# Kernel tuning notes

Hardware: AMD Instinct MI355X
Metric: run time of the kernel (lower is better)

The kernel has to match this reference:

```python
import jax, jax.numpy as jnp
import numpy as np

IN_FF = 7  # joints
MASK = np.ones(9, dtype=np.float32)  # [P(3), RPY sin/cos (6)]


def _mlp(x, params):
    # params: list of (W, b); sigmoid after every layer except the last (predict)
    h = x
    for W, b in params[:-1]:
        h = jax.nn.sigmoid(h @ W + b)
    W, b = params[-1]
    return h @ W + b


def _rpy_head(x, params):
    # FeedForwardNet_RPY forward: y -> [sin(y0), cos(y1)], angle = atan2(sin, cos)
    y = _mlp(x, params)
    s = jnp.sin(y[..., 0])
    c = jnp.cos(y[..., 1])
    ang = jnp.arctan2(s, c)
    return jnp.stack([s, c, ang], axis=-1)  # (..., 3)


def setup_inputs():
    key = jax.random.key(0)
    ks = jax.random.split(key, 26)
    m = 16384
    d = {"x": jax.random.normal(ks[0], (m, 2 * IN_FF), jnp.float32)}

    def lin(k, fi, fo, name, i):
        k1, k2 = jax.random.split(k)
        lim = 1.0 / np.sqrt(fi)  # torch Linear default init
        d[name + "_W" + str(i)] = jax.random.uniform(k1, (fi, fo), jnp.float32, -lim, lim)
        d[name + "_b" + str(i)] = jax.random.uniform(k2, (fo,), jnp.float32, -lim, lim)

    idx = 1
    for name, dims in [("pos", [7, 512, 512, 3]), ("roll", [7, 256, 256, 2]),
                       ("pitch", [7, 256, 256, 2]), ("yaw", [7, 256, 256, 2])]:
        for i in range(3):
            lin(ks[idx], dims[i], dims[i + 1], name, i)
            idx += 1
    return d


def _forward(x, pos_p, roll_p, pitch_p, yaw_p):
    mask = jnp.asarray(MASK)
    M_P, M_RPY = mask[:3], mask[3:]
    q, qdot = x[:, :IN_FF], x[:, IN_FF:]

    # position net: forward + per-sample Jacobian (exact, replaces the autograd loop)
    P = _mlp(q, pos_p)                                          # (m, 3)
    J_P = jax.vmap(jax.jacfwd(lambda z: _mlp(z, pos_p)))(q)     # (m, 3, 7)
    vel = jnp.einsum("moi,mi->mo", J_P, qdot)                   # bmm(J_P, jointVels)
    P = P * M_P
    vel = vel * M_P

    heads = []
    for p in (roll_p, pitch_p, yaw_p):
        f = lambda z, p=p: _rpy_head(z, p)
        y = f(q)                                # (m, 3): [sin, cos, angle]
        J = jax.vmap(jax.jacfwd(f))(q)          # (m, 3, 7)
        v = jnp.einsum("moi,mi->mo", J[:, :2, :], qdot)  # (m, 2)
        heads.append((y, J, v))
    (yR, JR, vR), (yPi, JPi, vPi), (yY, JY, vY) = heads

    # order: [roll_sin, pitch_sin, yaw_sin, roll_cos, pitch_cos, yaw_cos]
    RPY = jnp.stack([yR[:, 0], yPi[:, 0], yY[:, 0], yR[:, 1], yPi[:, 1], yY[:, 1]], axis=1) * M_RPY
    vel_RPY = jnp.stack([vR[:, 0], vPi[:, 0], vY[:, 0], vR[:, 1], vPi[:, 1], vY[:, 1]], axis=1) * M_RPY
    J_RPY = jnp.stack([JR[:, 0], JPi[:, 0], JY[:, 0], JR[:, 1], JPi[:, 1], JY[:, 1]], axis=1)  # (m,6,7)

    out = jnp.concatenate([P, RPY, vel, vel_RPY], axis=1)            # (m, 18)
    J_tot = jnp.concatenate([J_P, J_RPY], axis=1)                    # (m, 9, 7)
    out_angles = jnp.concatenate([P, yR[:, 2:3], yPi[:, 2:3], yY[:, 2:3]], axis=1)       # (m, 6)
    J_tot_angles = jnp.concatenate([J_P, JR[:, 2:3], JPi[:, 2:3], JY[:, 2:3]], axis=1)   # (m, 6, 7)
    return out, J_tot, out_angles, J_tot_angles


def reference(x, pos_W0, pos_b0, pos_W1, pos_b1, pos_W2, pos_b2,
              roll_W0, roll_b0, roll_W1, roll_b1, roll_W2, roll_b2,
              pitch_W0, pitch_b0, pitch_W1, pitch_b1, pitch_W2, pitch_b2,
              yaw_W0, yaw_b0, yaw_W1, yaw_b1, yaw_W2, yaw_b2):
    pos_p = [(pos_W0, pos_b0), (pos_W1, pos_b1), (pos_W2, pos_b2)]
    roll_p = [(roll_W0, roll_b0), (roll_W1, roll_b1), (roll_W2, roll_b2)]
    pitch_p = [(pitch_W0, pitch_b0), (pitch_W1, pitch_b1), (pitch_W2, pitch_b2)]
    yaw_p = [(yaw_W0, yaw_b0), (yaw_W1, yaw_b1), (yaw_W2, yaw_b2)]
    return _forward(x, pos_p, roll_p, pitch_p, yaw_p)
```

## Files before the change

kernel.cpp:

```cpp
#include <hip/hip_runtime.h>
#include <math.h>

typedef __attribute__((ext_vector_type(8))) short short8;
typedef __attribute__((ext_vector_type(4))) float floatx4;

__device__ __forceinline__ float sig(float z) {
    return __builtin_amdgcn_rcpf(1.0f + __expf(-z));
}

__device__ __forceinline__ unsigned short f2bf(float f) {
    unsigned u = __float_as_uint(f);
    u = (u + 0x7FFFu + ((u >> 16) & 1u)) >> 16;
    return (unsigned short)u;
}

#if __has_builtin(__builtin_amdgcn_cvt_pk_bf16_f32)
typedef __attribute__((ext_vector_type(2))) short short2v;
__device__ __forceinline__ unsigned int pack2bf(float a, float b) {
    short2v r = __builtin_amdgcn_cvt_pk_bf16_f32(a, b);
    return *(unsigned int*)&r;
}
#else
__device__ __forceinline__ unsigned int pack2bf(float a, float b) {
    unsigned ua = __float_as_uint(a), ub = __float_as_uint(b);
    ua += 0x7FFFu + ((ua >> 16) & 1u);
    ub += 0x7FFFu + ((ub >> 16) & 1u);
    return __builtin_amdgcn_perm(ub, ua, 0x07060302);
}
#endif

__global__ void convert_all(const float* __restrict__ s0, const float* __restrict__ s1,
                            const float* __restrict__ s2, const float* __restrict__ s3,
                            unsigned short* __restrict__ ws) {
    int idx = blockIdx.x * 256 + threadIdx.x;
    const float* src; unsigned short* dst; int H, logH, local;
    if (idx < 262144) { src = s0; dst = ws; H = 512; logH = 9; local = idx; }
    else {
        int r = idx - 262144; int m = r >> 16; local = r & 65535;
        H = 256; logH = 8;
        src = (m == 0) ? s1 : (m == 1) ? s2 : s3;
        dst = ws + 262144 + m * 65536;
    }
    int n = local & (H - 1), k = local >> logH;
    int KT = H >> 5;
    int blk = (n >> 4) * KT + (k >> 5);
    int lane = ((k >> 3) & 3) * 16 + (n & 15);
    int j = k & 7;
    dst[(blk * 64 + lane) * 8 + j] = f2bf(src[local]);
}

struct PosS {
    float B0[512], B1[512], W2[1536];
    float Q[8][8], Qd[8][8];
    float Acc[4][64][3], Sum[64][3];
};
struct RpyS {
    float B0[256], B1[256], W2[512];
    float Q[16][8], Qd[16][8];
    float Acc[4][128][2], Sum[128][2];
};

__global__ __launch_bounds__(256, 2)
void fused_mfma(const float* __restrict__ x,
                const float* __restrict__ pW0, const float* __restrict__ pb0,
                const float* __restrict__ pb1,
                const float* __restrict__ pW2, const float* __restrict__ pb2,
                const float* __restrict__ rW0_, const float* __restrict__ rb0_,
                const float* __restrict__ rb1_,
                const float* __restrict__ rW2_, const float* __restrict__ rb2_,
                const float* __restrict__ piW0, const float* __restrict__ pib0,
                const float* __restrict__ pib1,
                const float* __restrict__ piW2, const float* __restrict__ pib2,
                const float* __restrict__ yW0, const float* __restrict__ yb0,
                const float* __restrict__ yb1,
                const float* __restrict__ yW2, const float* __restrict__ yb2,
                const unsigned short* __restrict__ wsBase,
                float* __restrict__ out, int ns)
{
    extern __shared__ unsigned short sA[];
    __shared__ union { PosS p; RpyS r; } sU;

    const int tid = threadIdx.x;
    const int f = blockIdx.x;
    const int g = f / 5, r5 = f % 5;
    const size_t JTOT = (size_t)ns * 18, OUTA = (size_t)ns * 81, JANG = (size_t)ns * 87;
    const floatx4 z4 = {0.f, 0.f, 0.f, 0.f};
    const int w = tid >> 6, lane = tid & 63;
    const int quad = lane >> 4, col = lane & 15;
    const int srcl = lane & 47;

    if (r5 < 2) {
        const int m0 = (g * 2 + r5) * 8;
        const unsigned short* wsW1 = wsBase;

        if (tid < 128) {
            ((float4*)sU.p.B0)[tid] = ((const float4*)pb0)[tid];
            ((float4*)sU.p.B1)[tid] = ((const float4*)pb1)[tid];
        }
        for (int i = tid; i < 384; i += 256) ((float4*)sU.p.W2)[i] = ((const float4*)pW2)[i];
        if (tid < 112) {
            int m = tid / 14, c = tid % 14;
            float v = x[(m0 + m) * 14 + c];
            if (c < 7) sU.p.Q[m][c] = v; else sU.p.Qd[m][c - 7] = v;
        }
        __syncthreads();

        const float4* W04 = (const float4*)pW0;
        #pragma unroll
        for (int t = 0; t < 2; ++t) {
            int item = tid + t * 256;
            int s = item >> 6, k8 = item & 63;
            float q[7], w0v[7][8];
            #pragma unroll
            for (int i = 0; i < 7; i++) {
                q[i] = sU.p.Q[s][i];
                float4 a = W04[i * 128 + k8 * 2], b4 = W04[i * 128 + k8 * 2 + 1];
                w0v[i][0]=a.x; w0v[i][1]=a.y; w0v[i][2]=a.z; w0v[i][3]=a.w;
                w0v[i][4]=b4.x; w0v[i][5]=b4.y; w0v[i][6]=b4.z; w0v[i][7]=b4.w;
            }
            float hv[8], dv[8];
            #pragma unroll
            for (int jj = 0; jj < 8; jj++) {
                float z = sU.p.B0[k8 * 8 + jj];
                #pragma unroll
                for (int i = 0; i < 7; i++) z = fmaf(q[i], w0v[i][jj], z);
                float h = sig(z);
                hv[jj] = h; dv[jj] = h - h * h;
            }
            int kt = k8 >> 2, kq = k8 & 3, sw = kt & 7;
            int rr0 = s * 8;
            {
                uint4 v;
                v.x = pack2bf(hv[0], hv[1]); v.y = pack2bf(hv[2], hv[3]);
                v.z = pack2bf(hv[4], hv[5]); v.w = pack2bf(hv[6], hv[7]);
                *(uint4*)&sA[((rr0 >> 4) * 16 + kt) * 512 + ((kq * 16 + (rr0 & 15)) ^ sw) * 8] = v;
            }
            #pragma unroll
            for (int i = 0; i < 7; i++) {
                int rr = rr0 + 1 + i;
                uint4 v;
                v.x = pack2bf(dv[0] * w0v[i][0], dv[1] * w0v[i][1]);
                v.y = pack2bf(dv[2] * w0v[i][2], dv[3] * w0v[i][3]);
                v.z = pack2bf(dv[4] * w0v[i][4], dv[5] * w0v[i][5]);
                v.w = pack2bf(dv[6] * w0v[i][6], dv[7] * w0v[i][7]);
                *(uint4*)&sA[((rr >> 4) * 16 + kt) * 512 + ((kq * 16 + (rr & 15)) ^ sw) * 8] = v;
            }
        }
        __syncthreads();

        floatx4 acc[4][8];
        #pragma unroll
        for (int rt = 0; rt < 4; rt++)
            #pragma unroll
            for (int ct = 0; ct < 8; ct++) acc[rt][ct] = z4;

        const short8* bbase = (const short8*)wsW1 + (size_t)(w * 8 * 16) * 64 + lane;
        short8 bufA[8], bufB[8];
        #pragma unroll
        for (int ct = 0; ct < 8; ++ct) bufA[ct] = bbase[(ct * 16) * 64];

        for (int kt2 = 0; kt2 < 16; kt2 += 2) {
            #pragma unroll
            for (int ct = 0; ct < 8; ++ct) bufB[ct] = bbase[(ct * 16 + kt2 + 1) * 64];
            {
                const int kt = kt2, sw = kt & 7;
                short8 afr[4];
                #pragma unroll
                for (int rt = 0; rt < 4; ++rt)
                    afr[rt] = *(const short8*)&sA[(rt * 16 + kt) * 512 + (lane ^ sw) * 8];
                #pragma unroll
                for (int ct = 0; ct < 8; ++ct)
                    #pragma unroll
                    for (int rt = 0; rt < 4; ++rt)
                        acc[rt][ct] = __builtin_amdgcn_mfma_f32_16x16x32_bf16(afr[rt], bufA[ct], acc[rt][ct], 0, 0, 0);
            }
            if (kt2 + 2 < 16) {
                #pragma unroll
                for (int ct = 0; ct < 8; ++ct) bufA[ct] = bbase[(ct * 16 + kt2 + 2) * 64];
            }
            {
                const int kt = kt2 + 1, sw = kt & 7;
                short8 afr[4];
                #pragma unroll
                for (int rt = 0; rt < 4; ++rt)
                    afr[rt] = *(const short8*)&sA[(rt * 16 + kt) * 512 + (lane ^ sw) * 8];
                #pragma unroll
                for (int ct = 0; ct < 8; ++ct)
                    #pragma unroll
                    for (int rt = 0; rt < 4; ++rt)
                        acc[rt][ct] = __builtin_amdgcn_mfma_f32_16x16x32_bf16(afr[rt], bufB[ct], acc[rt][ct], 0, 0, 0);
            }
        }

        float ep[4][4][3];
        #pragma unroll
        for (int a = 0; a < 4; a++) for (int b = 0; b < 4; b++) for (int c = 0; c < 3; c++) ep[a][b][c] = 0.f;

        #pragma unroll
        for (int ct = 0; ct < 8; ++ct) {
            const int n = w * 128 + ct * 16 + col;
            const float b1n = sU.p.B1[n];
            const float w20 = sU.p.W2[n * 3], w21 = sU.p.W2[n * 3 + 1], w22 = sU.p.W2[n * 3 + 2];
            #pragma unroll
            for (int rt = 0; rt < 4; ++rt) {
                float z2c = __shfl(acc[rt][ct][0], srcl);
                float h2 = sig(z2c + b1n);
                float d2 = h2 - h2 * h2;
                #pragma unroll
                for (int r = 0; r < 4; ++r) {
                    float gg = ((quad & 1) == 0 && r == 0) ? h2 : d2 * acc[rt][ct][r];
                    ep[rt][r][0] = fmaf(gg, w20, ep[rt][r][0]);
                    ep[rt][r][1] = fmaf(gg, w21, ep[rt][r][1]);
                    ep[rt][r][2] = fmaf(gg, w22, ep[rt][r][2]);
                }
            }
        }

        #pragma unroll
        for (int mask = 1; mask <= 8; mask <<= 1)
            #pragma unroll
            for (int a = 0; a < 4; a++)
                #pragma unroll
                for (int b = 0; b < 4; b++)
                    #pragma unroll
                    for (int c = 0; c < 3; c++)
                        ep[a][b][c] += __shfl_xor(ep[a][b][c], mask);
        if (col == 0) {
            #pragma unroll
            for (int rt = 0; rt < 4; ++rt)
                #pragma unroll
                for (int r = 0; r < 4; ++r) {
                    int row = rt * 16 + quad * 4 + r;
                    sU.p.Acc[w][row][0] = ep[rt][r][0];
                    sU.p.Acc[w][row][1] = ep[rt][r][1];
                    sU.p.Acc[w][row][2] = ep[rt][r][2];
                }
        }
        __syncthreads();

        if (tid < 192) {
            int row = tid / 3, j = tid % 3;
            float v = sU.p.Acc[0][row][j] + sU.p.Acc[1][row][j] + sU.p.Acc[2][row][j] + sU.p.Acc[3][row][j];
            int s = row >> 3, i = row & 7;
            size_t M = m0 + s;
            if (i == 0) { v += pb2[j]; out[M * 18 + j] = v; out[OUTA + M * 6 + j] = v; }
            else        { out[JTOT + M * 63 + j * 7 + (i - 1)] = v;
                          out[JANG + M * 42 + j * 7 + (i - 1)] = v; }
            sU.p.Sum[row][j] = v;
        }
        __syncthreads();
        if (tid < 24) {
            int s = tid / 3, j = tid % 3;
            float vel = 0.f;
            #pragma unroll
            for (int i = 0; i < 7; i++) vel = fmaf(sU.p.Sum[s * 8 + 1 + i][j], sU.p.Qd[s][i], vel);
            out[(size_t)(m0 + s) * 18 + 9 + j] = vel;
        }
    } else {
        const int h = r5 - 2;
        const int m0 = g * 16;
        const float* W0 = (h == 0) ? rW0_ : (h == 1) ? piW0 : yW0;
        const float* b0 = (h == 0) ? rb0_ : (h == 1) ? pib0 : yb0;
        const float* b1 = (h == 0) ? rb1_ : (h == 1) ? pib1 : yb1;
        const float* W2 = (h == 0) ? rW2_ : (h == 1) ? piW2 : yW2;
        const float* b2 = (h == 0) ? rb2_ : (h == 1) ? pib2 : yb2;
        const unsigned short* wsW1 = wsBase + 262144 + h * 65536;

        if (tid < 64) {
            ((float4*)sU.r.B0)[tid] = ((const float4*)b0)[tid];
            ((float4*)sU.r.B1)[tid] = ((const float4*)b1)[tid];
        } else if (tid < 192) {
            ((float4*)sU.r.W2)[tid - 64] = ((const float4*)W2)[tid - 64];
        }
        if (tid < 224) {
            int m = tid / 14, c = tid % 14;
            float v = x[(m0 + m) * 14 + c];
            if (c < 7) sU.r.Q[m][c] = v; else sU.r.Qd[m][c - 7] = v;
        }
        __syncthreads();

        const float4* W04 = (const float4*)W0;
        #pragma unroll
        for (int t = 0; t < 2; ++t) {
            int item = tid + t * 256;
            int s = item >> 5, k8 = item & 31;
            float q[7], w0v[7][8];
            #pragma unroll
            for (int i = 0; i < 7; i++) {
                q[i] = sU.r.Q[s][i];
                float4 a = W04[i * 64 + k8 * 2], b4 = W04[i * 64 + k8 * 2 + 1];
                w0v[i][0]=a.x; w0v[i][1]=a.y; w0v[i][2]=a.z; w0v[i][3]=a.w;
                w0v[i][4]=b4.x; w0v[i][5]=b4.y; w0v[i][6]=b4.z; w0v[i][7]=b4.w;
            }
            float hv[8], dv[8];
            #pragma unroll
            for (int jj = 0; jj < 8; jj++) {
                float z = sU.r.B0[k8 * 8 + jj];
                #pragma unroll
                for (int i = 0; i < 7; i++) z = fmaf(q[i], w0v[i][jj], z);
                float hh = sig(z);
                hv[jj] = hh; dv[jj] = hh - hh * hh;
            }
            int kt = k8 >> 2, kq = k8 & 3, sw = kt & 7;
            int rr0 = s * 8;
            {
                uint4 v;
                v.x = pack2bf(hv[0], hv[1]); v.y = pack2bf(hv[2], hv[3]);
                v.z = pack2bf(hv[4], hv[5]); v.w = pack2bf(hv[6], hv[7]);
                *(uint4*)&sA[((rr0 >> 4) * 8 + kt) * 512 + ((kq * 16 + (rr0 & 15)) ^ sw) * 8] = v;
            }
            #pragma unroll
            for (int i = 0; i < 7; i++) {
                int rr = rr0 + 1 + i;
                uint4 v;
                v.x = pack2bf(dv[0] * w0v[i][0], dv[1] * w0v[i][1]);
                v.y = pack2bf(dv[2] * w0v[i][2], dv[3] * w0v[i][3]);
                v.z = pack2bf(dv[4] * w0v[i][4], dv[5] * w0v[i][5]);
                v.w = pack2bf(dv[6] * w0v[i][6], dv[7] * w0v[i][7]);
                *(uint4*)&sA[((rr >> 4) * 8 + kt) * 512 + ((kq * 16 + (rr & 15)) ^ sw) * 8] = v;
            }
        }
        __syncthreads();

        floatx4 acc[8][4];
        #pragma unroll
        for (int rt = 0; rt < 8; rt++)
            #pragma unroll
            for (int ct = 0; ct < 4; ct++) acc[rt][ct] = z4;

        const short8* bbase = (const short8*)wsW1 + (size_t)(w * 4 * 8) * 64 + lane;
        short8 bufA[4], bufB[4];
        #pragma unroll
        for (int ct = 0; ct < 4; ++ct) bufA[ct] = bbase[(ct * 8) * 64];

        for (int kt2 = 0; kt2 < 8; kt2 += 2) {
            #pragma unroll
            for (int ct = 0; ct < 4; ++ct) bufB[ct] = bbase[(ct * 8 + kt2 + 1) * 64];
            {
                const int kt = kt2, sw = kt & 7;
                short8 afr[8];
                #pragma unroll
                for (int rt = 0; rt < 8; ++rt)
                    afr[rt] = *(const short8*)&sA[(rt * 8 + kt) * 512 + (lane ^ sw) * 8];
                #pragma unroll
                for (int ct = 0; ct < 4; ++ct)
                    #pragma unroll
                    for (int rt = 0; rt < 8; ++rt)
                        acc[rt][ct] = __builtin_amdgcn_mfma_f32_16x16x32_bf16(afr[rt], bufA[ct], acc[rt][ct], 0, 0, 0);
            }
            if (kt2 + 2 < 8) {
                #pragma unroll
                for (int ct = 0; ct < 4; ++ct) bufA[ct] = bbase[(ct * 8 + kt2 + 2) * 64];
            }
            {
                const int kt = kt2 + 1, sw = kt & 7;
                short8 afr[8];
                #pragma unroll
                for (int rt = 0; rt < 8; ++rt)
                    afr[rt] = *(const short8*)&sA[(rt * 8 + kt) * 512 + (lane ^ sw) * 8];
                #pragma unroll
                for (int ct = 0; ct < 4; ++ct)
                    #pragma unroll
                    for (int rt = 0; rt < 8; ++rt)
                        acc[rt][ct] = __builtin_amdgcn_mfma_f32_16x16x32_bf16(afr[rt], bufB[ct], acc[rt][ct], 0, 0, 0);
            }
        }

        float ep[8][4][2];
        #pragma unroll
        for (int a = 0; a < 8; a++) for (int b = 0; b < 4; b++) for (int c = 0; c < 2; c++) ep[a][b][c] = 0.f;

        #pragma unroll
        for (int ct = 0; ct < 4; ++ct) {
            const int n = w * 64 + ct * 16 + col;
            const float b1n = sU.r.B1[n];
            const float w20 = sU.r.W2[n * 2], w21 = sU.r.W2[n * 2 + 1];
            #pragma unroll
            for (int rt = 0; rt < 8; ++rt) {
                float z2c = __shfl(acc[rt][ct][0], srcl);
                float h2 = sig(z2c + b1n);
                float d2 = h2 - h2 * h2;
                #pragma unroll
                for (int r = 0; r < 4; ++r) {
                    float gg = ((quad & 1) == 0 && r == 0) ? h2 : d2 * acc[rt][ct][r];
                    ep[rt][r][0] = fmaf(gg, w20, ep[rt][r][0]);
                    ep[rt][r][1] = fmaf(gg, w21, ep[rt][r][1]);
                }
            }
        }

        #pragma unroll
        for (int mask = 1; mask <= 8; mask <<= 1)
            #pragma unroll
            for (int a = 0; a < 8; a++)
                #pragma unroll
                for (int b = 0; b < 4; b++)
                    #pragma unroll
                    for (int c = 0; c < 2; c++)
                        ep[a][b][c] += __shfl_xor(ep[a][b][c], mask);
        if (col == 0) {
            #pragma unroll
            for (int rt = 0; rt < 8; ++rt)
                #pragma unroll
                for (int r = 0; r < 4; ++r) {
                    int row = rt * 16 + quad * 4 + r;
                    sU.r.Acc[w][row][0] = ep[rt][r][0];
                    sU.r.Acc[w][row][1] = ep[rt][r][1];
                }
        }
        __syncthreads();

        if (tid < 256) {
            int row = tid >> 1, j = tid & 1;
            float v = sU.r.Acc[0][row][j] + sU.r.Acc[1][row][j] + sU.r.Acc[2][row][j] + sU.r.Acc[3][row][j];
            if ((row & 7) == 0) v += b2[j];
            sU.r.Sum[row][j] = v;
        }
        __syncthreads();

        if (tid < 16) {
            int s = tid;
            size_t M = m0 + s;
            float y0 = sU.r.Sum[s * 8][0], y1 = sU.r.Sum[s * 8][1];
            float sv = sinf(y0), cv = cosf(y1);
            out[M * 18 + 3 + h] = sv;
            out[M * 18 + 6 + h] = cv;
            out[OUTA + M * 6 + 3 + h] = atan2f(sv, cv);
            float f0 = cosf(y0), f1 = -sinf(y1);
            float inv = __builtin_amdgcn_rcpf(fmaf(sv, sv, cv * cv));
            float v0 = 0.f, v1 = 0.f;
            #pragma unroll
            for (int i = 0; i < 7; i++) {
                float r0 = f0 * sU.r.Sum[s * 8 + 1 + i][0];
                float r1 = f1 * sU.r.Sum[s * 8 + 1 + i][1];
                out[JTOT + M * 63 + (3 + h) * 7 + i] = r0;
                out[JTOT + M * 63 + (6 + h) * 7 + i] = r1;
                out[JANG + M * 42 + (3 + h) * 7 + i] = (cv * r0 - sv * r1) * inv;
                v0 = fmaf(r0, sU.r.Qd[s][i], v0);
                v1 = fmaf(r1, sU.r.Qd[s][i], v1);
            }
            out[M * 18 + 12 + h] = v0;
            out[M * 18 + 15 + h] = v1;
        }
    }
}

extern "C" void kernel_launch(void* const* d_in, const int* in_sizes, int n_in,
                              void* d_out, int out_size, void* d_ws, size_t ws_size,
                              hipStream_t stream) {
    (void)n_in; (void)out_size; (void)ws_size;
    const float* x = (const float*)d_in[0];
    float* out = (float*)d_out;
    unsigned short* ws = (unsigned short*)d_ws;
    const int ns = in_sizes[0] / 14;

    convert_all<<<dim3(1792), 256, 0, stream>>>(
        (const float*)d_in[3], (const float*)d_in[9],
        (const float*)d_in[15], (const float*)d_in[21], ws);

    fused_mfma<<<dim3((ns / 8 / 2) * 5), 256, 65536, stream>>>(
        x,
        (const float*)d_in[1],  (const float*)d_in[2],  (const float*)d_in[4],
        (const float*)d_in[5],  (const float*)d_in[6],
        (const float*)d_in[7],  (const float*)d_in[8],  (const float*)d_in[10],
        (const float*)d_in[11], (const float*)d_in[12],
        (const float*)d_in[13], (const float*)d_in[14], (const float*)d_in[16],
        (const float*)d_in[17], (const float*)d_in[18],
        (const float*)d_in[19], (const float*)d_in[20], (const float*)d_in[22],
        (const float*)d_in[23], (const float*)d_in[24],
        ws, out, ns);
}
```

Measured before the change: 341.7 us.

## Process two sample tiles per block with double-buffered inputs, read W2 from global

Each block now loops over two consecutive sample tiles instead of one, halving the grid and amortising per-block setup (bias loads) across tiles. The next tile's input rows are prefetched into a second shared buffer while the current tile's MFMA loop runs. The W2 staging in shared memory is dropped, and the epilogue now reads W2 directly from global memory. The trade-off is fewer blocks in flight and serialised tile work per block, plus possible extra global latency in the epilogue.

```diff
diff --git a/kernel.cpp b/kernel.cpp
--- a/kernel.cpp
+++ b/kernel.cpp
@@ -50,13 +50,13 @@
 }
 
 struct PosS {
-    float B0[512], B1[512], W2[1536];
-    float Q[8][8], Qd[8][8];
+    float B0[512], B1[512];
+    float Qx[2][8][16];
     float Acc[4][64][3], Sum[64][3];
 };
 struct RpyS {
-    float B0[256], B1[256], W2[512];
-    float Q[16][8], Qd[16][8];
+    float B0[256], B1[256];
+    float Qx[2][16][16];
     float Acc[4][128][2], Sum[128][2];
 };
 
@@ -90,175 +90,175 @@
     const int srcl = lane & 47;
 
     if (r5 < 2) {
-        const int m0 = (g * 2 + r5) * 8;
+        const int m_base = g * 32 + r5 * 16;
         const unsigned short* wsW1 = wsBase;
 
         if (tid < 128) {
             ((float4*)sU.p.B0)[tid] = ((const float4*)pb0)[tid];
             ((float4*)sU.p.B1)[tid] = ((const float4*)pb1)[tid];
         }
-        for (int i = tid; i < 384; i += 256) ((float4*)sU.p.W2)[i] = ((const float4*)pW2)[i];
         if (tid < 112) {
             int m = tid / 14, c = tid % 14;
-            float v = x[(m0 + m) * 14 + c];
-            if (c < 7) sU.p.Q[m][c] = v; else sU.p.Qd[m][c - 7] = v;
+            sU.p.Qx[0][m][c] = x[((size_t)m_base + m) * 14 + c];
         }
         __syncthreads();
 
         const float4* W04 = (const float4*)pW0;
-        #pragma unroll
-        for (int t = 0; t < 2; ++t) {
-            int item = tid + t * 256;
-            int s = item >> 6, k8 = item & 63;
-            float q[7], w0v[7][8];
-            #pragma unroll
-            for (int i = 0; i < 7; i++) {
-                q[i] = sU.p.Q[s][i];
-                float4 a = W04[i * 128 + k8 * 2], b4 = W04[i * 128 + k8 * 2 + 1];
-                w0v[i][0]=a.x; w0v[i][1]=a.y; w0v[i][2]=a.z; w0v[i][3]=a.w;
-                w0v[i][4]=b4.x; w0v[i][5]=b4.y; w0v[i][6]=b4.z; w0v[i][7]=b4.w;
-            }
-            float hv[8], dv[8];
-            #pragma unroll
-            for (int jj = 0; jj < 8; jj++) {
-                float z = sU.p.B0[k8 * 8 + jj];
-                #pragma unroll
-                for (int i = 0; i < 7; i++) z = fmaf(q[i], w0v[i][jj], z);
-                float h = sig(z);
-                hv[jj] = h; dv[jj] = h - h * h;
-            }
-            int kt = k8 >> 2, kq = k8 & 3, sw = kt & 7;
-            int rr0 = s * 8;
-            {
-                uint4 v;
-                v.x = pack2bf(hv[0], hv[1]); v.y = pack2bf(hv[2], hv[3]);
-                v.z = pack2bf(hv[4], hv[5]); v.w = pack2bf(hv[6], hv[7]);
-                *(uint4*)&sA[((rr0 >> 4) * 16 + kt) * 512 + ((kq * 16 + (rr0 & 15)) ^ sw) * 8] = v;
-            }
-            #pragma unroll
-            for (int i = 0; i < 7; i++) {
-                int rr = rr0 + 1 + i;
-                uint4 v;
-                v.x = pack2bf(dv[0] * w0v[i][0], dv[1] * w0v[i][1]);
-                v.y = pack2bf(dv[2] * w0v[i][2], dv[3] * w0v[i][3]);
-                v.z = pack2bf(dv[4] * w0v[i][4], dv[5] * w0v[i][5]);
-                v.w = pack2bf(dv[6] * w0v[i][6], dv[7] * w0v[i][7]);
-                *(uint4*)&sA[((rr >> 4) * 16 + kt) * 512 + ((kq * 16 + (rr & 15)) ^ sw) * 8] = v;
-            }
-        }
-        __syncthreads();
-
-        floatx4 acc[4][8];
-        #pragma unroll
-        for (int rt = 0; rt < 4; rt++)
-            #pragma unroll
-            for (int ct = 0; ct < 8; ct++) acc[rt][ct] = z4;
-
-        const short8* bbase = (const short8*)wsW1 + (size_t)(w * 8 * 16) * 64 + lane;
-        short8 bufA[8], bufB[8];
-        #pragma unroll
-        for (int ct = 0; ct < 8; ++ct) bufA[ct] = bbase[(ct * 16) * 64];
-
-        for (int kt2 = 0; kt2 < 16; kt2 += 2) {
-            #pragma unroll
-            for (int ct = 0; ct < 8; ++ct) bufB[ct] = bbase[(ct * 16 + kt2 + 1) * 64];
-            {
-                const int kt = kt2, sw = kt & 7;
-                short8 afr[4];
+        for (int st = 0; st < 2; ++st) {
+            const int m0 = m_base + st * 8;
+            const int buf = st & 1;
+            #pragma unroll
+            for (int t = 0; t < 2; ++t) {
+                int item = tid + t * 256;
+                int s = item >> 6, k8 = item & 63;
+                float q[7], w0v[7][8];
+                #pragma unroll
+                for (int i = 0; i < 7; i++) {
+                    q[i] = sU.p.Qx[buf][s][i];
+                    float4 a = W04[i * 128 + k8 * 2], b4 = W04[i * 128 + k8 * 2 + 1];
+                    w0v[i][0]=a.x; w0v[i][1]=a.y; w0v[i][2]=a.z; w0v[i][3]=a.w;
+                    w0v[i][4]=b4.x; w0v[i][5]=b4.y; w0v[i][6]=b4.z; w0v[i][7]=b4.w;
+                }
+                float hv[8], dv[8];
+                #pragma unroll
+                for (int jj = 0; jj < 8; jj++) {
+                    float z = sU.p.B0[k8 * 8 + jj];
+                    #pragma unroll
+                    for (int i = 0; i < 7; i++) z = fmaf(q[i], w0v[i][jj], z);
+                    float h = sig(z);
+                    hv[jj] = h; dv[jj] = h - h * h;
+                }
+                int kt = k8 >> 2, kq = k8 & 3, sw = kt & 7;
+                int rr0 = s * 8;
+                {
+                    uint4 v;
+                    v.x = pack2bf(hv[0], hv[1]); v.y = pack2bf(hv[2], hv[3]);
+                    v.z = pack2bf(hv[4], hv[5]); v.w = pack2bf(hv[6], hv[7]);
+                    *(uint4*)&sA[((rr0 >> 4) * 16 + kt) * 512 + ((kq * 16 + (rr0 & 15)) ^ sw) * 8] = v;
+                }
+                #pragma unroll
+                for (int i = 0; i < 7; i++) {
+                    int rr = rr0 + 1 + i;
+                    uint4 v;
+                    v.x = pack2bf(dv[0] * w0v[i][0], dv[1] * w0v[i][1]);
+                    v.y = pack2bf(dv[2] * w0v[i][2], dv[3] * w0v[i][3]);
+                    v.z = pack2bf(dv[4] * w0v[i][4], dv[5] * w0v[i][5]);
+                    v.w = pack2bf(dv[6] * w0v[i][6], dv[7] * w0v[i][7]);
+                    *(uint4*)&sA[((rr >> 4) * 16 + kt) * 512 + ((kq * 16 + (rr & 15)) ^ sw) * 8] = v;
+                }
+            }
+            __syncthreads();
+            if (st + 1 < 2 && tid < 112) {
+                int m = tid / 14, c = tid % 14;
+                sU.p.Qx[1][m][c] = x[((size_t)m_base + 8 + m) * 14 + c];
+            }
+            floatx4 acc[4][8];
+            #pragma unroll
+            for (int rt = 0; rt < 4; rt++)
+                #pragma unroll
+                for (int ct = 0; ct < 8; ct++) acc[rt][ct] = z4;
+
+            const short8* bbase = (const short8*)wsW1 + (size_t)(w * 8 * 16) * 64 + lane;
+            short8 bufA[8], bufB[8];
+            #pragma unroll
+            for (int ct = 0; ct < 8; ++ct) bufA[ct] = bbase[(ct * 16) * 64];
+            for (int kt2 = 0; kt2 < 16; kt2 += 2) {
+                #pragma unroll
+                for (int ct = 0; ct < 8; ++ct) bufB[ct] = bbase[(ct * 16 + kt2 + 1) * 64];
+                {
+                    const int kt = kt2, sw = kt & 7;
+                    short8 afr[4];
+                    #pragma unroll
+                    for (int rt = 0; rt < 4; ++rt)
+                        afr[rt] = *(const short8*)&sA[(rt * 16 + kt) * 512 + (lane ^ sw) * 8];
+                    #pragma unroll
+                    for (int ct = 0; ct < 8; ++ct)
+                        #pragma unroll
+                        for (int rt = 0; rt < 4; ++rt)
+                            acc[rt][ct] = __builtin_amdgcn_mfma_f32_16x16x32_bf16(afr[rt], bufA[ct], acc[rt][ct], 0, 0, 0);
+                }
+                if (kt2 + 2 < 16) {
+                    #pragma unroll
+                    for (int ct = 0; ct < 8; ++ct) bufA[ct] = bbase[(ct * 16 + kt2 + 2) * 64];
+                }
+                {
+                    const int kt = kt2 + 1, sw = kt & 7;
+                    short8 afr[4];
+                    #pragma unroll
+                    for (int rt = 0; rt < 4; ++rt)
+                        afr[rt] = *(const short8*)&sA[(rt * 16 + kt) * 512 + (lane ^ sw) * 8];
+                    #pragma unroll
+                    for (int ct = 0; ct < 8; ++ct)
+                        #pragma unroll
+                        for (int rt = 0; rt < 4; ++rt)
+                            acc[rt][ct] = __builtin_amdgcn_mfma_f32_16x16x32_bf16(afr[rt], bufB[ct], acc[rt][ct], 0, 0, 0);
+                }
+            }
+            float ep[4][4][3];
+            #pragma unroll
+            for (int a = 0; a < 4; a++) for (int b = 0; b < 4; b++) for (int c = 0; c < 3; c++) ep[a][b][c] = 0.f;
+            #pragma unroll
+            for (int ct = 0; ct < 8; ++ct) {
+                const int n = w * 128 + ct * 16 + col;
+                const float b1n = sU.p.B1[n];
+                const float w20 = pW2[n * 3], w21 = pW2[n * 3 + 1], w22 = pW2[n * 3 + 2];
+                #pragma unroll
+                for (int rt = 0; rt < 4; ++rt) {
+                    float z2c = __shfl(acc[rt][ct][0], srcl);
+                    float h2 = sig(z2c + b1n);
+                    float d2 = h2 - h2 * h2;
+                    #pragma unroll
+                    for (int r = 0; r < 4; ++r) {
+                        float gg = ((quad & 1) == 0 && r == 0) ? h2 : d2 * acc[rt][ct][r];
+                        ep[rt][r][0] = fmaf(gg, w20, ep[rt][r][0]);
+                        ep[rt][r][1] = fmaf(gg, w21, ep[rt][r][1]);
+                        ep[rt][r][2] = fmaf(gg, w22, ep[rt][r][2]);
+                    }
+                }
+            }
+            #pragma unroll
+            for (int mask = 1; mask <= 8; mask <<= 1)
+                #pragma unroll
+                for (int a = 0; a < 4; a++)
+                    #pragma unroll
+                    for (int b = 0; b < 4; b++)
+                        #pragma unroll
+                        for (int c = 0; c < 3; c++)
+                            ep[a][b][c] += __shfl_xor(ep[a][b][c], mask);
+            if (col == 0) {
                 #pragma unroll
                 for (int rt = 0; rt < 4; ++rt)
-                    afr[rt] = *(const short8*)&sA[(rt * 16 + kt) * 512 + (lane ^ sw) * 8];
-                #pragma unroll
-                for (int ct = 0; ct < 8; ++ct)
-                    #pragma unroll
-                    for (int rt = 0; rt < 4; ++rt)
-                        acc[rt][ct] = __builtin_amdgcn_mfma_f32_16x16x32_bf16(afr[rt], bufA[ct], acc[rt][ct], 0, 0, 0);
-            }
-            if (kt2 + 2 < 16) {
-                #pragma unroll
-                for (int ct = 0; ct < 8; ++ct) bufA[ct] = bbase[(ct * 16 + kt2 + 2) * 64];
-            }
-            {
-                const int kt = kt2 + 1, sw = kt & 7;
-                short8 afr[4];
-                #pragma unroll
-                for (int rt = 0; rt < 4; ++rt)
-                    afr[rt] = *(const short8*)&sA[(rt * 16 + kt) * 512 + (lane ^ sw) * 8];
-                #pragma unroll
-                for (int ct = 0; ct < 8; ++ct)
-                    #pragma unroll
-                    for (int rt = 0; rt < 4; ++rt)
-                        acc[rt][ct] = __builtin_amdgcn_mfma_f32_16x16x32_bf16(afr[rt], bufB[ct], acc[rt][ct], 0, 0, 0);
-            }
-        }
-
-        float ep[4][4][3];
-        #pragma unroll
-        for (int a = 0; a < 4; a++) for (int b = 0; b < 4; b++) for (int c = 0; c < 3; c++) ep[a][b][c] = 0.f;
-
-        #pragma unroll
-        for (int ct = 0; ct < 8; ++ct) {
-            const int n = w * 128 + ct * 16 + col;
-            const float b1n = sU.p.B1[n];
-            const float w20 = sU.p.W2[n * 3], w21 = sU.p.W2[n * 3 + 1], w22 = sU.p.W2[n * 3 + 2];
-            #pragma unroll
-            for (int rt = 0; rt < 4; ++rt) {
-                float z2c = __shfl(acc[rt][ct][0], srcl);
-                float h2 = sig(z2c + b1n);
-                float d2 = h2 - h2 * h2;
-                #pragma unroll
-                for (int r = 0; r < 4; ++r) {
-                    float gg = ((quad & 1) == 0 && r == 0) ? h2 : d2 * acc[rt][ct][r];
-                    ep[rt][r][0] = fmaf(gg, w20, ep[rt][r][0]);
-                    ep[rt][r][1] = fmaf(gg, w21, ep[rt][r][1]);
-                    ep[rt][r][2] = fmaf(gg, w22, ep[rt][r][2]);
-                }
-            }
-        }
-
-        #pragma unroll
-        for (int mask = 1; mask <= 8; mask <<= 1)
-            #pragma unroll
-            for (int a = 0; a < 4; a++)
-                #pragma unroll
-                for (int b = 0; b < 4; b++)
-                    #pragma unroll
-                    for (int c = 0; c < 3; c++)
-                        ep[a][b][c] += __shfl_xor(ep[a][b][c], mask);
-        if (col == 0) {
-            #pragma unroll
-            for (int rt = 0; rt < 4; ++rt)
-                #pragma unroll
-                for (int r = 0; r < 4; ++r) {
-                    int row = rt * 16 + quad * 4 + r;
-                    sU.p.Acc[w][row][0] = ep[rt][r][0];
-                    sU.p.Acc[w][row][1] = ep[rt][r][1];
-                    sU.p.Acc[w][row][2] = ep[rt][r][2];
-                }
-        }
-        __syncthreads();
-
-        if (tid < 192) {
-            int row = tid / 3, j = tid % 3;
-            float v = sU.p.Acc[0][row][j] + sU.p.Acc[1][row][j] + sU.p.Acc[2][row][j] + sU.p.Acc[3][row][j];
-            int s = row >> 3, i = row & 7;
-            size_t M = m0 + s;
-            if (i == 0) { v += pb2[j]; out[M * 18 + j] = v; out[OUTA + M * 6 + j] = v; }
-            else        { out[JTOT + M * 63 + j * 7 + (i - 1)] = v;
-                          out[JANG + M * 42 + j * 7 + (i - 1)] = v; }
-            sU.p.Sum[row][j] = v;
-        }
-        __syncthreads();
-        if (tid < 24) {
-            int s = tid / 3, j = tid % 3;
-            float vel = 0.f;
-            #pragma unroll
-            for (int i = 0; i < 7; i++) vel = fmaf(sU.p.Sum[s * 8 + 1 + i][j], sU.p.Qd[s][i], vel);
-            out[(size_t)(m0 + s) * 18 + 9 + j] = vel;
+                    #pragma unroll
+                    for (int r = 0; r < 4; ++r) {
+                        int row = rt * 16 + quad * 4 + r;
+                        sU.p.Acc[w][row][0] = ep[rt][r][0];
+                        sU.p.Acc[w][row][1] = ep[rt][r][1];
+                        sU.p.Acc[w][row][2] = ep[rt][r][2];
+                    }
+            }
+            __syncthreads();
+            if (tid < 192) {
+                int row = tid / 3, j = tid % 3;
+                float v = sU.p.Acc[0][row][j] + sU.p.Acc[1][row][j] + sU.p.Acc[2][row][j] + sU.p.Acc[3][row][j];
+                int s = row >> 3, i = row & 7;
+                size_t M = m0 + s;
+                if (i == 0) { v += pb2[j]; out[M * 18 + j] = v; out[OUTA + M * 6 + j] = v; }
+                else        { out[JTOT + M * 63 + j * 7 + (i - 1)] = v;
+                              out[JANG + M * 42 + j * 7 + (i - 1)] = v; }
+                sU.p.Sum[row][j] = v;
+            }
+            __syncthreads();
+            if (tid < 24) {
+                int s = tid / 3, j = tid % 3;
+                float vel = 0.f;
+                #pragma unroll
+                for (int i = 0; i < 7; i++) vel = fmaf(sU.p.Sum[s * 8 + 1 + i][j], sU.p.Qx[buf][s][7 + i], vel);
+                out[(size_t)(m0 + s) * 18 + 9 + j] = vel;
+            }
         }
     } else {
         const int h = r5 - 2;
-        const int m0 = g * 16;
+        const int m_base = g * 32;
         const float* W0 = (h == 0) ? rW0_ : (h == 1) ? piW0 : yW0;
         const float* b0 = (h == 0) ? rb0_ : (h == 1) ? pib0 : yb0;
         const float* b1 = (h == 0) ? rb1_ : (h == 1) ? pib1 : yb1;
@@ -269,178 +269,176 @@
         if (tid < 64) {
             ((float4*)sU.r.B0)[tid] = ((const float4*)b0)[tid];
             ((float4*)sU.r.B1)[tid] = ((const float4*)b1)[tid];
-        } else if (tid < 192) {
-            ((float4*)sU.r.W2)[tid - 64] = ((const float4*)W2)[tid - 64];
         }
         if (tid < 224) {
             int m = tid / 14, c = tid % 14;
-            float v = x[(m0 + m) * 14 + c];
-            if (c < 7) sU.r.Q[m][c] = v; else sU.r.Qd[m][c - 7] = v;
+            sU.r.Qx[0][m][c] = x[((size_t)m_base + m) * 14 + c];
         }
         __syncthreads();
 
         const float4* W04 = (const float4*)W0;
-        #pragma unroll
-        for (int t = 0; t < 2; ++t) {
-            int item = tid + t * 256;
-            int s = item >> 5, k8 = item & 31;
-            float q[7], w0v[7][8];
-            #pragma unroll
-            for (int i = 0; i < 7; i++) {
-                q[i] = sU.r.Q[s][i];
-                float4 a = W04[i * 64 + k8 * 2], b4 = W04[i * 64 + k8 * 2 + 1];
-                w0v[i][0]=a.x; w0v[i][1]=a.y; w0v[i][2]=a.z; w0v[i][3]=a.w;
-                w0v[i][4]=b4.x; w0v[i][5]=b4.y; w0v[i][6]=b4.z; w0v[i][7]=b4.w;
-            }
-            float hv[8], dv[8];
-            #pragma unroll
-            for (int jj = 0; jj < 8; jj++) {
-                float z = sU.r.B0[k8 * 8 + jj];
-                #pragma unroll
-                for (int i = 0; i < 7; i++) z = fmaf(q[i], w0v[i][jj], z);
-                float hh = sig(z);
-                hv[jj] = hh; dv[jj] = hh - hh * hh;
-            }
-            int kt = k8 >> 2, kq = k8 & 3, sw = kt & 7;
-            int rr0 = s * 8;
-            {
-                uint4 v;
-                v.x = pack2bf(hv[0], hv[1]); v.y = pack2bf(hv[2], hv[3]);
-                v.z = pack2bf(hv[4], hv[5]); v.w = pack2bf(hv[6], hv[7]);
-                *(uint4*)&sA[((rr0 >> 4) * 8 + kt) * 512 + ((kq * 16 + (rr0 & 15)) ^ sw) * 8] = v;
-            }
-            #pragma unroll
-            for (int i = 0; i < 7; i++) {
-                int rr = rr0 + 1 + i;
-                uint4 v;
-                v.x = pack2bf(dv[0] * w0v[i][0], dv[1] * w0v[i][1]);
-                v.y = pack2bf(dv[2] * w0v[i][2], dv[3] * w0v[i][3]);
-                v.z = pack2bf(dv[4] * w0v[i][4], dv[5] * w0v[i][5]);
-                v.w = pack2bf(dv[6] * w0v[i][6], dv[7] * w0v[i][7]);
-                *(uint4*)&sA[((rr >> 4) * 8 + kt) * 512 + ((kq * 16 + (rr & 15)) ^ sw) * 8] = v;
-            }
-        }
-        __syncthreads();
-
-        floatx4 acc[8][4];
-        #pragma unroll
-        for (int rt = 0; rt < 8; rt++)
-            #pragma unroll
-            for (int ct = 0; ct < 4; ct++) acc[rt][ct] = z4;
-
-        const short8* bbase = (const short8*)wsW1 + (size_t)(w * 4 * 8) * 64 + lane;
-        short8 bufA[4], bufB[4];
-        #pragma unroll
-        for (int ct = 0; ct < 4; ++ct) bufA[ct] = bbase[(ct * 8) * 64];
-
-        for (int kt2 = 0; kt2 < 8; kt2 += 2) {
-            #pragma unroll
-            for (int ct = 0; ct < 4; ++ct) bufB[ct] = bbase[(ct * 8 + kt2 + 1) * 64];
-            {
-                const int kt = kt2, sw = kt & 7;
-                short8 afr[8];
+        for (int st = 0; st < 2; ++st) {
+            const int m0 = m_base + st * 16;
+            const int buf = st & 1;
+            #pragma unroll
+            for (int t = 0; t < 2; ++t) {
+                int item = tid + t * 256;
+                int s = item >> 5, k8 = item & 31;
+                float q[7], w0v[7][8];
+                #pragma unroll
+                for (int i = 0; i < 7; i++) {
+                    q[i] = sU.r.Qx[buf][s][i];
+                    float4 a = W04[i * 64 + k8 * 2], b4 = W04[i * 64 + k8 * 2 + 1];
+                    w0v[i][0]=a.x; w0v[i][1]=a.y; w0v[i][2]=a.z; w0v[i][3]=a.w;
+                    w0v[i][4]=b4.x; w0v[i][5]=b4.y; w0v[i][6]=b4.z; w0v[i][7]=b4.w;
+                }
+                float hv[8], dv[8];
+                #pragma unroll
+                for (int jj = 0; jj < 8; jj++) {
+                    float z = sU.r.B0[k8 * 8 + jj];
+                    #pragma unroll
+                    for (int i = 0; i < 7; i++) z = fmaf(q[i], w0v[i][jj], z);
+                    float hh = sig(z);
+                    hv[jj] = hh; dv[jj] = hh - hh * hh;
+                }
+                int kt = k8 >> 2, kq = k8 & 3, sw = kt & 7;
+                int rr0 = s * 8;
+                {
+                    uint4 v;
+                    v.x = pack2bf(hv[0], hv[1]); v.y = pack2bf(hv[2], hv[3]);
+                    v.z = pack2bf(hv[4], hv[5]); v.w = pack2bf(hv[6], hv[7]);
+                    *(uint4*)&sA[((rr0 >> 4) * 8 + kt) * 512 + ((kq * 16 + (rr0 & 15)) ^ sw) * 8] = v;
+                }
+                #pragma unroll
+                for (int i = 0; i < 7; i++) {
+                    int rr = rr0 + 1 + i;
+                    uint4 v;
+                    v.x = pack2bf(dv[0] * w0v[i][0], dv[1] * w0v[i][1]);
+                    v.y = pack2bf(dv[2] * w0v[i][2], dv[3] * w0v[i][3]);
+                    v.z = pack2bf(dv[4] * w0v[i][4], dv[5] * w0v[i][5]);
+                    v.w = pack2bf(dv[6] * w0v[i][6], dv[7] * w0v[i][7]);
+                    *(uint4*)&sA[((rr >> 4) * 8 + kt) * 512 + ((kq * 16 + (rr & 15)) ^ sw) * 8] = v;
+                }
+            }
+            __syncthreads();
+            if (st + 1 < 2 && tid < 224) {
+                int m = tid / 14, c = tid % 14;
+                sU.r.Qx[1][m][c] = x[((size_t)m_base + 16 + m) * 14 + c];
+            }
+            floatx4 acc[8][4];
+            #pragma unroll
+            for (int rt = 0; rt < 8; rt++)
+                #pragma unroll
+                for (int ct = 0; ct < 4; ct++) acc[rt][ct] = z4;
+
+            const short8* bbase = (const short8*)wsW1 + (size_t)(w * 4 * 8) * 64 + lane;
+            short8 bufA[4], bufB[4];
+            #pragma unroll
+            for (int ct = 0; ct < 4; ++ct) bufA[ct] = bbase[(ct * 8) * 64];
+            for (int kt2 = 0; kt2 < 8; kt2 += 2) {
+                #pragma unroll
+                for (int ct = 0; ct < 4; ++ct) bufB[ct] = bbase[(ct * 8 + kt2 + 1) * 64];
+                {
+                    const int kt = kt2, sw = kt & 7;
+                    short8 afr[8];
+                    #pragma unroll
+                    for (int rt = 0; rt < 8; ++rt)
+                        afr[rt] = *(const short8*)&sA[(rt * 8 + kt) * 512 + (lane ^ sw) * 8];
+                    #pragma unroll
+                    for (int ct = 0; ct < 4; ++ct)
+                        #pragma unroll
+                        for (int rt = 0; rt < 8; ++rt)
+                            acc[rt][ct] = __builtin_amdgcn_mfma_f32_16x16x32_bf16(afr[rt], bufA[ct], acc[rt][ct], 0, 0, 0);
+                }
+                if (kt2 + 2 < 8) {
+                    #pragma unroll
+                    for (int ct = 0; ct < 4; ++ct) bufA[ct] = bbase[(ct * 8 + kt2 + 2) * 64];
+                }
+                {
+                    const int kt = kt2 + 1, sw = kt & 7;
+                    short8 afr[8];
+                    #pragma unroll
+                    for (int rt = 0; rt < 8; ++rt)
+                        afr[rt] = *(const short8*)&sA[(rt * 8 + kt) * 512 + (lane ^ sw) * 8];
+                    #pragma unroll
+                    for (int ct = 0; ct < 4; ++ct)
+                        #pragma unroll
+                        for (int rt = 0; rt < 8; ++rt)
+                            acc[rt][ct] = __builtin_amdgcn_mfma_f32_16x16x32_bf16(afr[rt], bufB[ct], acc[rt][ct], 0, 0, 0);
+                }
+            }
+            float ep[8][4][2];
+            #pragma unroll
+            for (int a = 0; a < 8; a++) for (int b = 0; b < 4; b++) for (int c = 0; c < 2; c++) ep[a][b][c] = 0.f;
+            #pragma unroll
+            for (int ct = 0; ct < 4; ++ct) {
+                const int n = w * 64 + ct * 16 + col;
+                const float b1n = sU.r.B1[n];
+                const float w20 = W2[n * 2], w21 = W2[n * 2 + 1];
+                #pragma unroll
+                for (int rt = 0; rt < 8; ++rt) {
+                    float z2c = __shfl(acc[rt][ct][0], srcl);
+                    float h2 = sig(z2c + b1n);
+                    float d2 = h2 - h2 * h2;
+                    #pragma unroll
+                    for (int r = 0; r < 4; ++r) {
+                        float gg = ((quad & 1) == 0 && r == 0) ? h2 : d2 * acc[rt][ct][r];
+                        ep[rt][r][0] = fmaf(gg, w20, ep[rt][r][0]);
+                        ep[rt][r][1] = fmaf(gg, w21, ep[rt][r][1]);
+                    }
+                }
+            }
+            #pragma unroll
+            for (int mask = 1; mask <= 8; mask <<= 1)
+                #pragma unroll
+                for (int a = 0; a < 8; a++)
+                    #pragma unroll
+                    for (int b = 0; b < 4; b++)
+                        #pragma unroll
+                        for (int c = 0; c < 2; c++)
+                            ep[a][b][c] += __shfl_xor(ep[a][b][c], mask);
+            if (col == 0) {
                 #pragma unroll
                 for (int rt = 0; rt < 8; ++rt)
-                    afr[rt] = *(const short8*)&sA[(rt * 8 + kt) * 512 + (lane ^ sw) * 8];
-                #pragma unroll
-                for (int ct = 0; ct < 4; ++ct)
-                    #pragma unroll
-                    for (int rt = 0; rt < 8; ++rt)
-                        acc[rt][ct] = __builtin_amdgcn_mfma_f32_16x16x32_bf16(afr[rt], bufA[ct], acc[rt][ct], 0, 0, 0);
-            }
-            if (kt2 + 2 < 8) {
-                #pragma unroll
-                for (int ct = 0; ct < 4; ++ct) bufA[ct] = bbase[(ct * 8 + kt2 + 2) * 64];
-            }
-            {
-                const int kt = kt2 + 1, sw = kt & 7;
-                short8 afr[8];
-                #pragma unroll
-                for (int rt = 0; rt < 8; ++rt)
-                    afr[rt] = *(const short8*)&sA[(rt * 8 + kt) * 512 + (lane ^ sw) * 8];
-                #pragma unroll
-                for (int ct = 0; ct < 4; ++ct)
-                    #pragma unroll
-                    for (int rt = 0; rt < 8; ++rt)
-                        acc[rt][ct] = __builtin_amdgcn_mfma_f32_16x16x32_bf16(afr[rt], bufB[ct], acc[rt][ct], 0, 0, 0);
-            }
-        }
-
-        float ep[8][4][2];
-        #pragma unroll
-        for (int a = 0; a < 8; a++) for (int b = 0; b < 4; b++) for (int c = 0; c < 2; c++) ep[a][b][c] = 0.f;
-
-        #pragma unroll
-        for (int ct = 0; ct < 4; ++ct) {
-            const int n = w * 64 + ct * 16 + col;
-            const float b1n = sU.r.B1[n];
-            const float w20 = sU.r.W2[n * 2], w21 = sU.r.W2[n * 2 + 1];
-            #pragma unroll
-            for (int rt = 0; rt < 8; ++rt) {
-                float z2c = __shfl(acc[rt][ct][0], srcl);
-                float h2 = sig(z2c + b1n);
-                float d2 = h2 - h2 * h2;
-                #pragma unroll
-                for (int r = 0; r < 4; ++r) {
-                    float gg = ((quad & 1) == 0 && r == 0) ? h2 : d2 * acc[rt][ct][r];
-                    ep[rt][r][0] = fmaf(gg, w20, ep[rt][r][0]);
-                    ep[rt][r][1] = fmaf(gg, w21, ep[rt][r][1]);
-                }
-            }
-        }
-
-        #pragma unroll
-        for (int mask = 1; mask <= 8; mask <<= 1)
-            #pragma unroll
-            for (int a = 0; a < 8; a++)
-                #pragma unroll
-                for (int b = 0; b < 4; b++)
-                    #pragma unroll
-                    for (int c = 0; c < 2; c++)
-                        ep[a][b][c] += __shfl_xor(ep[a][b][c], mask);
-        if (col == 0) {
-            #pragma unroll
-            for (int rt = 0; rt < 8; ++rt)
-                #pragma unroll
-                for (int r = 0; r < 4; ++r) {
-                    int row = rt * 16 + quad * 4 + r;
-                    sU.r.Acc[w][row][0] = ep[rt][r][0];
-                    sU.r.Acc[w][row][1] = ep[rt][r][1];
-                }
-        }
-        __syncthreads();
-
-        if (tid < 256) {
-            int row = tid >> 1, j = tid & 1;
-            float v = sU.r.Acc[0][row][j] + sU.r.Acc[1][row][j] + sU.r.Acc[2][row][j] + sU.r.Acc[3][row][j];
-            if ((row & 7) == 0) v += b2[j];
-            sU.r.Sum[row][j] = v;
-        }
-        __syncthreads();
-
-        if (tid < 16) {
-            int s = tid;
-            size_t M = m0 + s;
-            float y0 = sU.r.Sum[s * 8][0], y1 = sU.r.Sum[s * 8][1];
-            float sv = sinf(y0), cv = cosf(y1);
-            out[M * 18 + 3 + h] = sv;
-            out[M * 18 + 6 + h] = cv;
-            out[OUTA + M * 6 + 3 + h] = atan2f(sv, cv);
-            float f0 = cosf(y0), f1 = -sinf(y1);
-            float inv = __builtin_amdgcn_rcpf(fmaf(sv, sv, cv * cv));
-            float v0 = 0.f, v1 = 0.f;
-            #pragma unroll
-            for (int i = 0; i < 7; i++) {
-                float r0 = f0 * sU.r.Sum[s * 8 + 1 + i][0];
-                float r1 = f1 * sU.r.Sum[s * 8 + 1 + i][1];
-                out[JTOT + M * 63 + (3 + h) * 7 + i] = r0;
-                out[JTOT + M * 63 + (6 + h) * 7 + i] = r1;
-                out[JANG + M * 42 + (3 + h) * 7 + i] = (cv * r0 - sv * r1) * inv;
-                v0 = fmaf(r0, sU.r.Qd[s][i], v0);
-                v1 = fmaf(r1, sU.r.Qd[s][i], v1);
-            }
-            out[M * 18 + 12 + h] = v0;
-            out[M * 18 + 15 + h] = v1;
+                    #pragma unroll
+                    for (int r = 0; r < 4; ++r) {
+                        int row = rt * 16 + quad * 4 + r;
+                        sU.r.Acc[w][row][0] = ep[rt][r][0];
+                        sU.r.Acc[w][row][1] = ep[rt][r][1];
+                    }
+            }
+            __syncthreads();
+            if (tid < 256) {
+                int row = tid >> 1, j = tid & 1;
+                float v = sU.r.Acc[0][row][j] + sU.r.Acc[1][row][j] + sU.r.Acc[2][row][j] + sU.r.Acc[3][row][j];
+                if ((row & 7) == 0) v += b2[j];
+                sU.r.Sum[row][j] = v;
+            }
+            __syncthreads();
+            if (tid < 16) {
+                int s = tid;
+                size_t M = m0 + s;
+                float y0 = sU.r.Sum[s * 8][0], y1 = sU.r.Sum[s * 8][1];
+                float sv = sinf(y0), cv = cosf(y1);
+                out[M * 18 + 3 + h] = sv;
+                out[M * 18 + 6 + h] = cv;
+                out[OUTA + M * 6 + 3 + h] = atan2f(sv, cv);
+                float f0 = cosf(y0), f1 = -sinf(y1);
+                float inv = __builtin_amdgcn_rcpf(fmaf(sv, sv, cv * cv));
+                float v0 = 0.f, v1 = 0.f;
+                #pragma unroll
+                for (int i = 0; i < 7; i++) {
+                    float r0 = f0 * sU.r.Sum[s * 8 + 1 + i][0];
+                    float r1 = f1 * sU.r.Sum[s * 8 + 1 + i][1];
+                    out[JTOT + M * 63 + (3 + h) * 7 + i] = r0;
+                    out[JTOT + M * 63 + (6 + h) * 7 + i] = r1;
+                    out[JANG + M * 42 + (3 + h) * 7 + i] = (cv * r0 - sv * r1) * inv;
+                    v0 = fmaf(r0, sU.r.Qx[buf][s][7 + i], v0);
+                    v1 = fmaf(r1, sU.r.Qx[buf][s][7 + i], v1);
+                }
+                out[M * 18 + 12 + h] = v0;
+                out[M * 18 + 15 + h] = v1;
+            }
         }
     }
 }
@@ -458,7 +456,7 @@
         (const float*)d_in[3], (const float*)d_in[9],
         (const float*)d_in[15], (const float*)d_in[21], ws);
 
-    fused_mfma<<<dim3((ns / 8 / 2) * 5), 256, 65536, stream>>>(
+    fused_mfma<<<dim3((ns / 32) * 5), 256, 65536, stream>>>(
         x,
         (const float*)d_in[1],  (const float*)d_in[2],  (const float*)d_in[4],
         (const float*)d_in[5],  (const float*)d_in[6],
```

Result: slower. 773.3 us (+126.3%).
